# Optimization experiments

Measured on AMD Instinct MI355X. Metric: run time of the kernel, lower is better.

Reference implementation:

```python
import jax, jax.numpy as jnp
import numpy as np

LAMBDA_L1 = 0.5
LAMBDA_SSIM = 0.5
ITERATIONS = 1000
THRESH = 0.01
SUB_N = 50000  # torch caps inlier-check set at 50k points


def setup_inputs() -> dict:
    key = jax.random.key(0)
    k1, k2 = jax.random.split(key)
    H, W = 1024, 2048  # Cityscapes resolution
    rendered_depth = jax.random.uniform(k1, (H, W), jnp.float32, 0.2, 10.0)
    prior_disparity = jax.random.uniform(k2, (H, W), jnp.float32, 0.0, 1.0)
    return {"rendered_depth": rendered_depth, "prior_disparity": prior_disparity}


def _ransac_linear_alignment(x, y, mask, key):
    """Fit y = s*x + t by RANSAC over masked points. x, y, mask are flat [P]."""
    P = x.shape[0]
    num_pts = mask.sum()
    # indices of masked points packed at the front (fixed-shape, jit-safe)
    idx_m = jnp.flatnonzero(mask, size=P, fill_value=0)
    k_pair, k_sub = jax.random.split(key)
    # random point pairs among the first num_pts (masked) entries
    pos = jax.random.randint(k_pair, (ITERATIONS, 2), 0, num_pts)
    pi = idx_m[pos]                                   # [iters, 2]
    x1, x2 = x[pi[:, 0]], x[pi[:, 1]]
    y1, y2 = y[pi[:, 0]], y[pi[:, 1]]
    scales = (y2 - y1) / (x2 - x1 + 1e-8)             # [iters]
    shifts = y1 - scales * x1                         # [iters]
    # subsample inlier-check set (with replacement; torch uses randperm)
    spos = jax.random.randint(k_sub, (SUB_N,), 0, num_pts)
    si = idx_m[spos]
    x_sub, y_sub = x[si], y[si]                       # [SUB_N]
    # dynamic threshold = 0.5 * MAD of masked y
    y_nan = jnp.where(mask, y, jnp.nan)
    med = jnp.nanmedian(y_nan)
    dyn = jnp.nanmedian(jnp.abs(y_nan - med)) * 0.5
    dyn = jnp.where(dyn < 1e-5, THRESH, dyn)
    # all iterations evaluated in parallel: [iters, SUB_N] residuals
    res = jnp.abs(scales[:, None] * x_sub[None, :] + shifts[:, None] - y_sub[None, :])
    counts = (res < dyn).sum(axis=1)
    counts = jnp.where(scales > 0, counts, -1)        # torch skips s <= 0
    best = jnp.argmax(counts)                         # first max == torch's strict-> update
    valid = counts[best] >= 0
    s = jnp.where(valid, scales[best], 1.0)
    t = jnp.where(valid, shifts[best], 0.0)
    # num_pts < 10 fallback
    s = jnp.where(num_pts < 10, 1.0, s)
    t = jnp.where(num_pts < 10, 0.0, t)
    return s, t


def reference(rendered_depth, prior_disparity):
    d_ren = rendered_depth
    d_pri = prior_disparity
    mask = (d_ren > 0.1) & (d_ren < 100.0) & jnp.isfinite(d_ren)
    target_inv_ren = 1.0 / (d_ren + 1e-6)
    n_valid = mask.sum()

    s, t = _ransac_linear_alignment(
        jax.lax.stop_gradient(d_pri).reshape(-1),
        jax.lax.stop_gradient(target_inv_ren).reshape(-1),
        mask.reshape(-1),
        jax.random.key(42),
    )
    aligned_prior_disp = s * d_pri + t
    # masked mean L1 (F.l1_loss over mask-selected elements)
    l1_loss = jnp.sum(jnp.abs(aligned_prior_disp - target_inv_ren) * mask) / jnp.maximum(n_valid, 1)
    total_loss = LAMBDA_L1 * l1_loss + LAMBDA_SSIM * 0.0  # ssim_module=None
    total_loss = jnp.where(n_valid < 100, 0.0, total_loss)  # early-exit branch
    prior_metric_depth = 1.0 / jnp.maximum(jax.lax.stop_gradient(aligned_prior_disp), 1e-4)
    return total_loss, target_inv_ren, prior_metric_depth
```

## Files before the change

### kernel.cpp

```cpp
#include <hip/hip_runtime.h>
#include <stdint.h>
#include <math.h>


#define NT 256
#define GA 128
#define GB 512
#define GC 128
#define GD 512
#define GE 256
#define GF 1024
#define LCAP 262144u

enum : uint32_t {
  W_CNT  = 0,
  W_LOSS = 4,
  W_N    = 6,
  W_VA   = 7, W_VB = 8,
  W_WA   = 9, W_WB = 10,
  W_SB1  = 12,
  W_SB2  = 16,
  W_COUNTS = 20,
  W_G1   = 1024,
  W_G2   = 17408,
  W_ZEND = 33792,
  W_PERC = 33792,
  W_SCALES = 34816,
  W_SHIFTS = 35816,
  W_XSUB = 36816,
  W_YSUB = 86816,
  W_LA1  = 136832,
  W_LB1  = W_LA1 + LCAP,
  W_LA2  = W_LB1 + LCAP,
  W_LB2  = W_LA2 + LCAP
};

__device__ __forceinline__ uint32_t rotl32(uint32_t v, int d) {
  return (v << d) | (v >> (32 - d));
}
__device__ __forceinline__ void tf2x32(uint32_t k0, uint32_t k1,
                                       uint32_t c0, uint32_t c1,
                                       uint32_t& o0, uint32_t& o1) {
  uint32_t ks2 = k0 ^ k1 ^ 0x1BD11BDAu;
  uint32_t x0 = c0 + k0;
  uint32_t x1 = c1 + k1;
#define TFR(r) { x0 += x1; x1 = rotl32(x1, r); x1 ^= x0; }
  TFR(13) TFR(15) TFR(26) TFR(6)
  x0 += k1;  x1 += ks2 + 1u;
  TFR(17) TFR(29) TFR(16) TFR(24)
  x0 += ks2; x1 += k0 + 2u;
  TFR(13) TFR(15) TFR(26) TFR(6)
  x0 += k0;  x1 += k1 + 3u;
  TFR(17) TFR(29) TFR(16) TFR(24)
  x0 += k1;  x1 += ks2 + 4u;
  TFR(13) TFR(15) TFR(26) TFR(6)
  x0 += ks2; x1 += k0 + 5u;
#undef TFR
  o0 = x0; o1 = x1;
}
struct Keys { uint32_t hp0, hp1, lp0, lp1, hs0, hs1, ls0, ls1; };
__device__ __forceinline__ Keys derive_keys() {
  Keys K; uint32_t p0, p1, q0, q1;
  tf2x32(0u, 42u, 0u, 0u, p0, p1);
  tf2x32(0u, 42u, 0u, 1u, q0, q1);
  tf2x32(p0, p1, 0u, 0u, K.hp0, K.hp1);
  tf2x32(p0, p1, 0u, 1u, K.lp0, K.lp1);
  tf2x32(q0, q1, 0u, 0u, K.hs0, K.hs1);
  tf2x32(q0, q1, 0u, 1u, K.ls0, K.ls1);
  return K;
}
__device__ __forceinline__ uint32_t bits32(uint32_t k0, uint32_t k1, uint32_t e) {
  uint32_t a, b; tf2x32(k0, k1, 0u, e, a, b); return a ^ b;
}
__device__ __forceinline__ uint32_t ri_offset(uint32_t hi, uint32_t lo, uint32_t span) {
  uint32_t m = 65536u % span;
  m = (m * m) % span;
  uint32_t off = (hi % span) * m + (lo % span);
  return off % span;
}

__device__ __forceinline__ uint32_t f2u(float f) {
  uint32_t u = __float_as_uint(f);
  return (u & 0x80000000u) ? ~u : (u | 0x80000000u);
}
__device__ __forceinline__ float u2f(uint32_t u) {
  uint32_t v = (u & 0x80000000u) ? (u & 0x7FFFFFFFu) : ~u;
  return __uint_as_float(v);
}
__device__ __forceinline__ uint32_t yval_u(float dv, float& y, bool& m) {
  y = __fdiv_rn(1.0f, __fadd_rn(dv, 1e-6f));
  m = (dv > 0.1f) && (dv < 100.0f) && isfinite(dv);
  return m ? f2u(y) : 0xFFFFFFFFu;
}
__device__ __forceinline__ uint32_t m2w(uint32_t u, float med) {
  return (u != 0xFFFFFFFFu) ? f2u(fabsf(__fsub_rn(u2f(u), med))) : 0xFFFFFFFFu;
}
__device__ __forceinline__ float med_from(const uint32_t* WS) {
  return __fmul_rn(__fadd_rn(u2f(WS[W_VA]), u2f(WS[W_VB])), 0.5f);
}

__device__ __forceinline__ uint32_t block_sum_u32(uint32_t v, uint32_t* wl) {
  const int lane = threadIdx.x & 63, wid = threadIdx.x >> 6;
  for (int off = 32; off > 0; off >>= 1) v += __shfl_down(v, off);
  __syncthreads();
  if (lane == 0) wl[wid] = v;
  __syncthreads();
  return wl[0] + wl[1] + wl[2] + wl[3];
}
__device__ __forceinline__ uint32_t scan_excl(uint32_t local, uint32_t* wl) {
  const int lane = threadIdx.x & 63, wid = threadIdx.x >> 6;
  __syncthreads();
  uint32_t v = local;
#pragma unroll
  for (int off = 1; off < 64; off <<= 1) {
    uint32_t o = __shfl_up(v, off);
    if (lane >= off) v += o;
  }
  if (lane == 63) wl[wid] = v;
  __syncthreads();
  uint32_t base = 0;
  for (int w = 0; w < 4; w++) if (w < wid) base += wl[w];
  return base + v - local;
}

__device__ void g_select2(const uint32_t* __restrict__ G, uint32_t rkA, uint32_t rkB,
                          uint32_t* wl, uint32_t* bc4) {
  const int tid = threadIdx.x;
  if (tid < 4) bc4[tid] = 0u;
  __syncthreads();
  uint32_t local = 0;
  for (int k = 0; k < 64; k++) local += G[tid * 64 + k];
  uint32_t excl = scan_excl(local, wl);
  for (int s = 0; s < 2; s++) {
    uint32_t rk = s ? rkB : rkA;
    if (local > 0 && rk >= excl && rk < excl + local) {
      uint32_t c = excl;
      for (int k = 0; k < 64; k++) {
        uint32_t v = G[tid * 64 + k];
        if (rk < c + v) { bc4[2 * s] = (uint32_t)(tid * 64 + k); bc4[2 * s + 1] = rk - c; break; }
        c += v;
      }
    }
  }
  __syncthreads();
}

__device__ uint32_t select17(const uint32_t* __restrict__ L, uint32_t cnt,
                             uint32_t rk, uint32_t bin14,
                             uint32_t* h512, uint32_t* h256,
                             uint32_t* wl, uint32_t* bc) {
  const int tid = threadIdx.x;
  __syncthreads();
  h512[2 * tid] = 0; h512[2 * tid + 1] = 0; h256[tid] = 0;
  if (tid < 2) bc[tid] = 0u;
  __syncthreads();
  for (uint32_t i = tid; i < cnt; i += NT)
    atomicAdd(&h512[(L[i] >> 8) & 511u], 1u);
  __syncthreads();
  uint32_t a0 = h512[2 * tid], a1 = h512[2 * tid + 1];
  uint32_t local = a0 + a1;
  uint32_t excl = scan_excl(local, wl);
  if (local > 0 && rk >= excl && rk < excl + local) {
    if (rk < excl + a0) { bc[0] = (uint32_t)(2 * tid); bc[1] = rk - excl; }
    else { bc[0] = (uint32_t)(2 * tid + 1); bc[1] = rk - excl - a0; }
  }
  __syncthreads();
  uint32_t binA = bc[0], rk2 = bc[1];
  __syncthreads();
  for (uint32_t i = tid; i < cnt; i += NT) {
    uint32_t v = L[i];
    if (((v >> 8) & 511u) == binA) atomicAdd(&h256[v & 255u], 1u);
  }
  __syncthreads();
  uint32_t l2 = h256[tid];
  uint32_t e2 = scan_excl(l2, wl);
  if (l2 > 0 && rk2 >= e2 && rk2 < e2 + l2) bc[0] = (uint32_t)tid;
  __syncthreads();
  uint32_t binB = bc[0];
  __syncthreads();
  return ((16384u + bin14) << 17) | (binA << 8) | binB;
}

__global__ void k_zero(uint32_t* WS) {
  int i = blockIdx.x * blockDim.x + threadIdx.x;
  if (i < (int)W_ZEND) WS[i] = 0u;
}

__global__ __launch_bounds__(NT) void kA(const float* __restrict__ dren,
                                         uint32_t* __restrict__ WS, int P) {
  const int tid = threadIdx.x, bid = blockIdx.x, gid = bid * NT + tid;
  __shared__ uint32_t lh[8192];
  __shared__ uint32_t wl[4];
  for (int i = tid; i < 8192; i += NT) lh[i] = 0u;
  __syncthreads();
  uint32_t cnt = 0;
  const float4* d4 = (const float4*)dren;
  const int P4 = P >> 2;
  for (int i = gid; i < P4; i += GA * NT) {
    float4 d = d4[i];
    float dc[4] = { d.x, d.y, d.z, d.w };
#pragma unroll
    for (int k = 0; k < 4; k++) {
      float y; bool m;
      uint32_t u = yval_u(dc[k], y, m);
      cnt += m ? 1u : 0u;
      uint32_t bin = (u >> 17) & 16383u;
      atomicAdd(&lh[bin >> 1], 1u << ((bin & 1u) << 4));
    }
  }
  for (int i = (P & ~3) + gid; i < P; i += GA * NT) {
    float y; bool m;
    uint32_t u = yval_u(dren[i], y, m);
    cnt += m ? 1u : 0u;
    uint32_t bin = (u >> 17) & 16383u;
    atomicAdd(&lh[bin >> 1], 1u << ((bin & 1u) << 4));
  }
  uint32_t btot = block_sum_u32(cnt, wl);
  if (tid == 0) WS[W_PERC + bid] = btot;
  __syncthreads();
  for (int w = tid; w < 8192; w += NT) {
    uint32_t pv = lh[w];
    if (pv) {
      uint32_t lo = pv & 0xFFFFu, hi = pv >> 16;
      if (lo) atomicAdd(&WS[W_G1 + 2 * w], lo);
      if (hi) atomicAdd(&WS[W_G1 + 2 * w + 1], hi);
    }
  }
}

__global__ __launch_bounds__(NT) void kB(const float* __restrict__ dren,
                                         const float* __restrict__ dpri,
                                         uint32_t* __restrict__ WS, int P) {
  const int tid = threadIdx.x, bid = blockIdx.x, gid = bid * NT + tid;
  __shared__ uint32_t bufA[4096], bufB[4096];
  __shared__ uint32_t cA, cB, baseA, baseB;
  __shared__ uint32_t wl[4], bc4[4];
  uint32_t local = (tid < GA) ? WS[W_PERC + tid] : 0u;
  const uint32_t n = block_sum_u32(local, wl);
  const uint32_t nn = n ? n : 1u;
  g_select2(WS + W_G1, (nn - 1u) >> 1, nn >> 1, wl, bc4);
  const uint32_t binA1 = bc4[0], binB1 = bc4[2];
  const bool dv1 = (binA1 != binB1);
  if (tid == 0) {
    WS[W_N] = n;
    WS[W_SB1 + 0] = bc4[0]; WS[W_SB1 + 1] = bc4[1];
    WS[W_SB1 + 2] = bc4[2]; WS[W_SB1 + 3] = bc4[3];
    cA = 0; cB = 0;
  }
  __syncthreads();
  {
    uint32_t span = n ? n : 1u;
    if (gid < 1000) {
      Keys K = derive_keys();
      uint32_t hi0 = bits32(K.hp0, K.hp1, (uint32_t)(2 * gid));
      uint32_t lo0 = bits32(K.lp0, K.lp1, (uint32_t)(2 * gid));
      uint32_t hi1 = bits32(K.hp0, K.hp1, (uint32_t)(2 * gid + 1));
      uint32_t lo1 = bits32(K.lp0, K.lp1, (uint32_t)(2 * gid + 1));
      uint32_t i0 = ri_offset(hi0, lo0, span);
      uint32_t i1 = ri_offset(hi1, lo1, span);
      float x1v = dpri[i0], x2v = dpri[i1];
      float y1v = __fdiv_rn(1.0f, __fadd_rn(dren[i0], 1e-6f));
      float y2v = __fdiv_rn(1.0f, __fadd_rn(dren[i1], 1e-6f));
      float sc = __fdiv_rn(__fsub_rn(y2v, y1v),
                           __fadd_rn(__fsub_rn(x2v, x1v), 1e-8f));
      ((float*)WS)[W_SCALES + gid] = sc;
      ((float*)WS)[W_SHIFTS + gid] = __fsub_rn(y1v, __fmul_rn(sc, x1v));
    }
    if (gid < 50000) {
      Keys K = derive_keys();
      uint32_t hi = bits32(K.hs0, K.hs1, (uint32_t)gid);
      uint32_t lo = bits32(K.ls0, K.ls1, (uint32_t)gid);
      uint32_t idx = ri_offset(hi, lo, span);
      ((float*)WS)[W_XSUB + gid] = dpri[idx];
      ((float*)WS)[W_YSUB + gid] = __fdiv_rn(1.0f, __fadd_rn(dren[idx], 1e-6f));
    }
  }
  const float4* d4 = (const float4*)dren;
  const int P4 = P >> 2;
  for (int i = gid; i < P4; i += GB * NT) {
    float4 d = d4[i];
    float dc[4] = { d.x, d.y, d.z, d.w };
#pragma unroll
    for (int k = 0; k < 4; k++) {
      float y; bool m;
      uint32_t u = yval_u(dc[k], y, m);
      uint32_t b = (u >> 17) & 16383u;
      if (b == binA1) { uint32_t j = atomicAdd(&cA, 1u); if (j < 4096u) bufA[j] = u; }
      else if (dv1 && b == binB1) { uint32_t j = atomicAdd(&cB, 1u); if (j < 4096u) bufB[j] = u; }
    }
  }
  for (int i = (P & ~3) + gid; i < P; i += GB * NT) {
    float y; bool m;
    uint32_t u = yval_u(dren[i], y, m);
    uint32_t b = (u >> 17) & 16383u;
    if (b == binA1) { uint32_t j = atomicAdd(&cA, 1u); if (j < 4096u) bufA[j] = u; }
    else if (dv1 && b == binB1) { uint32_t j = atomicAdd(&cB, 1u); if (j < 4096u) bufB[j] = u; }
  }
  __syncthreads();
  if (tid == 0) {
    uint32_t a = cA > 4096u ? 4096u : cA;
    uint32_t b = cB > 4096u ? 4096u : cB;
    cA = a; cB = b;
    baseA = a ? atomicAdd(&WS[W_CNT + 0], a) : 0u;
    baseB = b ? atomicAdd(&WS[W_CNT + 1], b) : 0u;
  }
  __syncthreads();
  for (uint32_t k = tid; k < cA; k += NT)
    if (baseA + k < LCAP) WS[W_LA1 + baseA + k] = bufA[k];
  for (uint32_t k = tid; k < cB; k += NT)
    if (baseB + k < LCAP) WS[W_LB1 + baseB + k] = bufB[k];
}

__global__ __launch_bounds__(NT) void kMed(uint32_t* __restrict__ WS) {
  const int bid = blockIdx.x;
  __shared__ uint32_t h512[512], h256[256];
  __shared__ uint32_t wl[4], bc[2];
  const uint32_t binA1 = WS[W_SB1 + 0], rkA1 = WS[W_SB1 + 1];
  const uint32_t binB1 = WS[W_SB1 + 2], rkB1 = WS[W_SB1 + 3];
  const bool dv1 = (binA1 != binB1);
  uint32_t bin, rk; const uint32_t* L; uint32_t cnt;
  if (bid == 0) {
    bin = binA1; rk = rkA1; L = WS + W_LA1;
    cnt = WS[W_CNT + 0];
  } else {
    bin = dv1 ? binB1 : binA1; rk = rkB1;
    L = dv1 ? (WS + W_LB1) : (WS + W_LA1);
    cnt = dv1 ? WS[W_CNT + 1] : WS[W_CNT + 0];
  }
  if (cnt > LCAP) cnt = LCAP;
  uint32_t v = select17(L, cnt, rk, bin, h512, h256, wl, bc);
  if (threadIdx.x == 0) WS[bid == 0 ? W_VA : W_VB] = v;
}

__global__ __launch_bounds__(NT) void kC(const float* __restrict__ dren,
                                         uint32_t* __restrict__ WS, int P) {
  const int tid = threadIdx.x, bid = blockIdx.x, gid = bid * NT + tid;
  __shared__ uint32_t lh[8192];
  const float med = med_from(WS);
  for (int i = tid; i < 8192; i += NT) lh[i] = 0u;
  __syncthreads();
  const float4* d4 = (const float4*)dren;
  const int P4 = P >> 2;
  for (int i = gid; i < P4; i += GC * NT) {
    float4 d = d4[i];
    float dc[4] = { d.x, d.y, d.z, d.w };
#pragma unroll
    for (int k = 0; k < 4; k++) {
      float y; bool m;
      uint32_t w = m2w(yval_u(dc[k], y, m), med);
      uint32_t bin = (w >> 17) & 16383u;
      atomicAdd(&lh[bin >> 1], 1u << ((bin & 1u) << 4));
    }
  }
  for (int i = (P & ~3) + gid; i < P; i += GC * NT) {
    float y; bool m;
    uint32_t w = m2w(yval_u(dren[i], y, m), med);
    uint32_t bin = (w >> 17) & 16383u;
    atomicAdd(&lh[bin >> 1], 1u << ((bin & 1u) << 4));
  }
  __syncthreads();
  for (int w = tid; w < 8192; w += NT) {
    uint32_t pv = lh[w];
    if (pv) {
      uint32_t lo = pv & 0xFFFFu, hi = pv >> 16;
      if (lo) atomicAdd(&WS[W_G2 + 2 * w], lo);
      if (hi) atomicAdd(&WS[W_G2 + 2 * w + 1], hi);
    }
  }
}

__global__ __launch_bounds__(NT) void kD(const float* __restrict__ dren,
                                         uint32_t* __restrict__ WS, int P) {
  const int tid = threadIdx.x, bid = blockIdx.x, gid = bid * NT + tid;
  __shared__ uint32_t bufA[4096], bufB[4096];
  __shared__ uint32_t cA, cB, baseA, baseB;
  __shared__ uint32_t wl[4], bc4[4];
  const float med = med_from(WS);
  const uint32_t n = WS[W_N];
  const uint32_t nn = n ? n : 1u;
  g_select2(WS + W_G2, (nn - 1u) >> 1, nn >> 1, wl, bc4);
  const uint32_t binA2 = bc4[0], binB2 = bc4[2];
  const bool dv2 = (binA2 != binB2);
  if (tid == 0) {
    WS[W_SB2 + 0] = bc4[0]; WS[W_SB2 + 1] = bc4[1];
    WS[W_SB2 + 2] = bc4[2]; WS[W_SB2 + 3] = bc4[3];
    cA = 0; cB = 0;
  }
  __syncthreads();
  const float4* d4 = (const float4*)dren;
  const int P4 = P >> 2;
  for (int i = gid; i < P4; i += GD * NT) {
    float4 d = d4[i];
    float dc[4] = { d.x, d.y, d.z, d.w };
#pragma unroll
    for (int k = 0; k < 4; k++) {
      float y; bool m;
      uint32_t w = m2w(yval_u(dc[k], y, m), med);
      uint32_t b = (w >> 17) & 16383u;
      if (b == binA2) { uint32_t j = atomicAdd(&cA, 1u); if (j < 4096u) bufA[j] = w; }
      else if (dv2 && b == binB2) { uint32_t j = atomicAdd(&cB, 1u); if (j < 4096u) bufB[j] = w; }
    }
  }
  for (int i = (P & ~3) + gid; i < P; i += GD * NT) {
    float y; bool m;
    uint32_t w = m2w(yval_u(dren[i], y, m), med);
    uint32_t b = (w >> 17) & 16383u;
    if (b == binA2) { uint32_t j = atomicAdd(&cA, 1u); if (j < 4096u) bufA[j] = w; }
    else if (dv2 && b == binB2) { uint32_t j = atomicAdd(&cB, 1u); if (j < 4096u) bufB[j] = w; }
  }
  __syncthreads();
  if (tid == 0) {
    uint32_t a = cA > 4096u ? 4096u : cA;
    uint32_t b = cB > 4096u ? 4096u : cB;
    cA = a; cB = b;
    baseA = a ? atomicAdd(&WS[W_CNT + 2], a) : 0u;
    baseB = b ? atomicAdd(&WS[W_CNT + 3], b) : 0u;
  }
  __syncthreads();
  for (uint32_t k = tid; k < cA; k += NT)
    if (baseA + k < LCAP) WS[W_LA2 + baseA + k] = bufA[k];
  for (uint32_t k = tid; k < cB; k += NT)
    if (baseB + k < LCAP) WS[W_LB2 + baseB + k] = bufB[k];
}

__global__ __launch_bounds__(NT) void kDyn(uint32_t* __restrict__ WS) {
  const int bid = blockIdx.x;
  __shared__ uint32_t h512[512], h256[256];
  __shared__ uint32_t wl[4], bc[2];
  const uint32_t binA2 = WS[W_SB2 + 0], rkA2 = WS[W_SB2 + 1];
  const uint32_t binB2 = WS[W_SB2 + 2], rkB2 = WS[W_SB2 + 3];
  const bool dv2 = (binA2 != binB2);
  uint32_t bin, rk; const uint32_t* L; uint32_t cnt;
  if (bid == 0) {
    bin = binA2; rk = rkA2; L = WS + W_LA2;
    cnt = WS[W_CNT + 2];
  } else {
    bin = dv2 ? binB2 : binA2; rk = rkB2;
    L = dv2 ? (WS + W_LB2) : (WS + W_LA2);
    cnt = dv2 ? WS[W_CNT + 3] : WS[W_CNT + 2];
  }
  if (cnt > LCAP) cnt = LCAP;
  uint32_t v = select17(L, cnt, rk, bin, h512, h256, wl, bc);
  if (threadIdx.x == 0) WS[bid == 0 ? W_WA : W_WB] = v;
}

__global__ __launch_bounds__(NT) void kE(uint32_t* __restrict__ WS) {
  const int tid = threadIdx.x, bid = blockIdx.x;
  __shared__ float lx[200], ly[200];
  float mad = __fmul_rn(__fadd_rn(u2f(WS[W_WA]), u2f(WS[W_WB])), 0.5f);
  float dyn = __fmul_rn(mad, 0.5f);
  if (dyn < 1e-5f) dyn = 0.01f;
  const int e0 = (bid * 50000) / GE, e1 = ((bid + 1) * 50000) / GE;
  const int cnt = e1 - e0;
  const float* x_sub = (const float*)WS + W_XSUB;
  const float* y_sub = (const float*)WS + W_YSUB;
  if (tid < cnt) { lx[tid] = x_sub[e0 + tid]; ly[tid] = y_sub[e0 + tid]; }
  __syncthreads();
  const float* scales = (const float*)WS + W_SCALES;
  const float* shifts = (const float*)WS + W_SHIFTS;
  float ss[4], tt[4]; int c[4];
#pragma unroll
  for (int j = 0; j < 4; j++) {
    int cand = tid + 256 * j;
    ss[j] = (cand < 1000) ? scales[cand] : 0.0f;
    tt[j] = (cand < 1000) ? shifts[cand] : 0.0f;
    c[j] = 0;
  }
  for (int e = 0; e < cnt; e++) {
    float xe = lx[e], ye = ly[e];
#pragma unroll
    for (int j = 0; j < 4; j++) {
      float r = fabsf(__fsub_rn(__fadd_rn(__fmul_rn(ss[j], xe), tt[j]), ye));
      c[j] += (r < dyn) ? 1 : 0;
    }
  }
  int* counts = (int*)WS + W_COUNTS;
#pragma unroll
  for (int j = 0; j < 4; j++) {
    int cand = tid + 256 * j;
    if (cand < 1000 && c[j] > 0) atomicAdd(&counts[cand], c[j]);
  }
}

__global__ __launch_bounds__(NT) void kF(const float* __restrict__ dren,
                                         const float* __restrict__ dpri,
                                         float* __restrict__ out,
                                         uint32_t* __restrict__ WS, int P) {
  const int tid = threadIdx.x, bid = blockIdx.x, gid = bid * NT + tid;
  const int lane = tid & 63, wid = tid >> 6;
  __shared__ int ired[4], iidx[4];
  __shared__ float fbcast[2];
  __shared__ double dred[4];
  {
    const int* counts = (const int*)WS + W_COUNTS;
    const float* scales = (const float*)WS + W_SCALES;
    const float* shifts = (const float*)WS + W_SHIFTS;
    int bcn = -2, bix = 0x7FFFFFFF;
    for (int j = tid; j < 1000; j += NT) {
      int cc = counts[j];
      if (!(scales[j] > 0.0f)) cc = -1;
      if (cc > bcn) { bcn = cc; bix = j; }
    }
    for (int off = 32; off > 0; off >>= 1) {
      int oc = __shfl_down(bcn, off), oi = __shfl_down(bix, off);
      if (oc > bcn || (oc == bcn && oi < bix)) { bcn = oc; bix = oi; }
    }
    if (lane == 0) { ired[wid] = bcn; iidx[wid] = bix; }
    __syncthreads();
    if (tid == 0) {
      for (int w = 1; w < 4; w++) {
        if (ired[w] > ired[0] || (ired[w] == ired[0] && iidx[w] < iidx[0])) {
          ired[0] = ired[w]; iidx[0] = iidx[w];
        }
      }
      bool valid = ired[0] >= 0;
      float s = valid ? scales[iidx[0]] : 1.0f;
      float t = valid ? shifts[iidx[0]] : 0.0f;
      uint32_t n = WS[W_N];
      if (n < 10u) { s = 1.0f; t = 0.0f; }
      fbcast[0] = s; fbcast[1] = t;
    }
    __syncthreads();
  }
  const float s = fbcast[0], t = fbcast[1];
  float* out_y = out + 1;
  float* out_depth = out + 1 + P;
  double acc = 0.0;
  const float4* d4 = (const float4*)dren;
  const float4* p4 = (const float4*)dpri;
  const int P4 = P >> 2;
  for (int i = gid; i < P4; i += GF * NT) {
    float4 d = d4[i], p = p4[i];
    float dc[4] = { d.x, d.y, d.z, d.w };
    float pc[4] = { p.x, p.y, p.z, p.w };
#pragma unroll
    for (int k = 0; k < 4; k++) {
      float yv = __fdiv_rn(1.0f, __fadd_rn(dc[k], 1e-6f));
      out_y[4 * i + k] = yv;
      float al = __fadd_rn(__fmul_rn(s, pc[k]), t);
      out_depth[4 * i + k] = __fdiv_rn(1.0f, fmaxf(al, 1e-4f));
      bool m = (dc[k] > 0.1f) && (dc[k] < 100.0f) && isfinite(dc[k]);
      if (m) acc += (double)fabsf(__fsub_rn(al, yv));
    }
  }
  for (int i = (P & ~3) + gid; i < P; i += GF * NT) {
    float dv = dren[i];
    float yv = __fdiv_rn(1.0f, __fadd_rn(dv, 1e-6f));
    out_y[i] = yv;
    float al = __fadd_rn(__fmul_rn(s, dpri[i]), t);
    out_depth[i] = __fdiv_rn(1.0f, fmaxf(al, 1e-4f));
    bool m = (dv > 0.1f) && (dv < 100.0f) && isfinite(dv);
    if (m) acc += (double)fabsf(__fsub_rn(al, yv));
  }
  for (int off = 32; off > 0; off >>= 1) acc += __shfl_down(acc, off);
  __syncthreads();
  if (lane == 0) dred[wid] = acc;
  __syncthreads();
  if (tid == 0)
    atomicAdd((double*)(WS + W_LOSS), dred[0] + dred[1] + dred[2] + dred[3]);
}

__global__ void kG(const uint32_t* __restrict__ WS, float* __restrict__ out) {
  if (threadIdx.x == 0 && blockIdx.x == 0) {
    double total = *((const double*)(WS + W_LOSS));
    uint32_t n = WS[W_N];
    uint32_t nd = n ? n : 1u;
    float l1 = __fdiv_rn((float)total, (float)nd);
    out[0] = (n < 100u) ? 0.0f : __fmul_rn(0.5f, l1);
  }
}

extern "C" void kernel_launch(void* const* d_in, const int* in_sizes, int n_in,
                              void* d_out, int out_size, void* d_ws, size_t ws_size,
                              hipStream_t stream) {
  const float* d_ren = (const float*)d_in[0];
  const float* d_pri = (const float*)d_in[1];
  float* out = (float*)d_out;
  uint32_t* WS = (uint32_t*)d_ws;
  int P = in_sizes[0];

  k_zero<<<(W_ZEND + NT - 1) / NT, NT, 0, stream>>>(WS);
  kA<<<GA, NT, 0, stream>>>(d_ren, WS, P);
  kB<<<GB, NT, 0, stream>>>(d_ren, d_pri, WS, P);
  kMed<<<2, NT, 0, stream>>>(WS);
  kC<<<GC, NT, 0, stream>>>(d_ren, WS, P);
  kD<<<GD, NT, 0, stream>>>(d_ren, WS, P);
  kDyn<<<2, NT, 0, stream>>>(WS);
  kE<<<GE, NT, 0, stream>>>(WS);
  kF<<<GF, NT, 0, stream>>>(d_ren, d_pri, out, WS, P);
  kG<<<1, 64, 0, stream>>>(WS, out);
}
```

Measured before the change: 226.2 us.

## Fuse median, MAD and final-loss kernels into last-block tails of producers

Removes the separate kMed, kDyn and kG launches. Each producer kernel (kB, kD, kF) now counts finished blocks with an atomic, and the last block to finish does the follow-up select or loss finalization. Writes use atomic exchange and reads use atomic loads, so the last block sees data written by the other blocks. This saves three launch gaps, but the two median selects now run one after another in a single block instead of two blocks in parallel.

Result: slower. 271.4 us (+20.0%).

```diff
diff --git a/kernel.cpp b/kernel.cpp
--- a/kernel.cpp
+++ b/kernel.cpp
@@ -16,10 +16,9 @@
   W_CNT  = 0,
   W_LOSS = 4,
   W_N    = 6,
-  W_VA   = 7, W_VB = 8,
-  W_WA   = 9, W_WB = 10,
-  W_SB1  = 12,
-  W_SB2  = 16,
+  W_MED  = 7,
+  W_DYN  = 8,
+  W_DONEB = 9, W_DONED = 10, W_DONEF = 11,
   W_COUNTS = 20,
   W_G1   = 1024,
   W_G2   = 17408,
@@ -95,8 +94,15 @@
 __device__ __forceinline__ uint32_t m2w(uint32_t u, float med) {
   return (u != 0xFFFFFFFFu) ? f2u(fabsf(__fsub_rn(u2f(u), med))) : 0xFFFFFFFFu;
 }
-__device__ __forceinline__ float med_from(const uint32_t* WS) {
-  return __fmul_rn(__fadd_rn(u2f(WS[W_VA]), u2f(WS[W_VB])), 0.5f);
+
+__device__ __forceinline__ uint32_t aload(const uint32_t* p) {
+  return __hip_atomic_load(p, __ATOMIC_RELAXED, __HIP_MEMORY_SCOPE_AGENT);
+}
+__device__ __forceinline__ uint32_t axchg(uint32_t* p, uint32_t v) {
+  return __hip_atomic_exchange(p, v, __ATOMIC_RELAXED, __HIP_MEMORY_SCOPE_AGENT);
+}
+__device__ __forceinline__ double aloadd(const double* p) {
+  return __hip_atomic_load(p, __ATOMIC_RELAXED, __HIP_MEMORY_SCOPE_AGENT);
 }
 
 __device__ __forceinline__ uint32_t block_sum_u32(uint32_t v, uint32_t* wl) {
@@ -145,17 +151,17 @@
   __syncthreads();
 }
 
-__device__ uint32_t select17(const uint32_t* __restrict__ L, uint32_t cnt,
-                             uint32_t rk, uint32_t bin14,
-                             uint32_t* h512, uint32_t* h256,
-                             uint32_t* wl, uint32_t* bc) {
+__device__ uint32_t select17a(const uint32_t* __restrict__ L, uint32_t cnt,
+                              uint32_t rk, uint32_t bin14,
+                              uint32_t* h512, uint32_t* h256,
+                              uint32_t* wl, uint32_t* bc) {
   const int tid = threadIdx.x;
   __syncthreads();
   h512[2 * tid] = 0; h512[2 * tid + 1] = 0; h256[tid] = 0;
   if (tid < 2) bc[tid] = 0u;
   __syncthreads();
   for (uint32_t i = tid; i < cnt; i += NT)
-    atomicAdd(&h512[(L[i] >> 8) & 511u], 1u);
+    atomicAdd(&h512[(aload(&L[i]) >> 8) & 511u], 1u);
   __syncthreads();
   uint32_t a0 = h512[2 * tid], a1 = h512[2 * tid + 1];
   uint32_t local = a0 + a1;
@@ -168,7 +174,7 @@
   uint32_t binA = bc[0], rk2 = bc[1];
   __syncthreads();
   for (uint32_t i = tid; i < cnt; i += NT) {
-    uint32_t v = L[i];
+    uint32_t v = aload(&L[i]);
     if (((v >> 8) & 511u) == binA) atomicAdd(&h256[v & 255u], 1u);
   }
   __syncthreads();
@@ -235,16 +241,17 @@
   __shared__ uint32_t bufA[4096], bufB[4096];
   __shared__ uint32_t cA, cB, baseA, baseB;
   __shared__ uint32_t wl[4], bc4[4];
+  __shared__ uint32_t h512[512], h256[256];
+  __shared__ int lastB;
   uint32_t local = (tid < GA) ? WS[W_PERC + tid] : 0u;
   const uint32_t n = block_sum_u32(local, wl);
   const uint32_t nn = n ? n : 1u;
   g_select2(WS + W_G1, (nn - 1u) >> 1, nn >> 1, wl, bc4);
-  const uint32_t binA1 = bc4[0], binB1 = bc4[2];
+  const uint32_t binA1 = bc4[0], rkA1 = bc4[1];
+  const uint32_t binB1 = bc4[2], rkB1 = bc4[3];
   const bool dv1 = (binA1 != binB1);
   if (tid == 0) {
     WS[W_N] = n;
-    WS[W_SB1 + 0] = bc4[0]; WS[W_SB1 + 1] = bc4[1];
-    WS[W_SB1 + 2] = bc4[2]; WS[W_SB1 + 3] = bc4[3];
     cA = 0; cB = 0;
   }
   __syncthreads();
@@ -305,38 +312,37 @@
     baseB = b ? atomicAdd(&WS[W_CNT + 1], b) : 0u;
   }
   __syncthreads();
+  uint32_t dummy = 1u;
   for (uint32_t k = tid; k < cA; k += NT)
-    if (baseA + k < LCAP) WS[W_LA1 + baseA + k] = bufA[k];
+    if (baseA + k < LCAP) dummy ^= axchg(&WS[W_LA1 + baseA + k], bufA[k]);
   for (uint32_t k = tid; k < cB; k += NT)
-    if (baseB + k < LCAP) WS[W_LB1 + baseB + k] = bufB[k];
-}
-
-__global__ __launch_bounds__(NT) void kMed(uint32_t* __restrict__ WS) {
-  const int bid = blockIdx.x;
-  __shared__ uint32_t h512[512], h256[256];
-  __shared__ uint32_t wl[4], bc[2];
-  const uint32_t binA1 = WS[W_SB1 + 0], rkA1 = WS[W_SB1 + 1];
-  const uint32_t binB1 = WS[W_SB1 + 2], rkB1 = WS[W_SB1 + 3];
-  const bool dv1 = (binA1 != binB1);
-  uint32_t bin, rk; const uint32_t* L; uint32_t cnt;
-  if (bid == 0) {
-    bin = binA1; rk = rkA1; L = WS + W_LA1;
-    cnt = WS[W_CNT + 0];
+    if (baseB + k < LCAP) dummy ^= axchg(&WS[W_LB1 + baseB + k], bufB[k]);
+  asm volatile("" :: "v"(dummy) : "memory");
+  __syncthreads();
+  if (tid == 0) {
+    uint32_t old = atomicAdd(&WS[W_DONEB], 1u);
+    lastB = (old == (uint32_t)(GB - 1)) ? 1 : 0;
+  }
+  __syncthreads();
+  if (!lastB) return;
+  uint32_t cA1 = aload(&WS[W_CNT + 0]); if (cA1 > LCAP) cA1 = LCAP;
+  uint32_t vA = select17a(WS + W_LA1, cA1, rkA1, binA1, h512, h256, wl, bc4);
+  uint32_t vB;
+  if (dv1) {
+    uint32_t cB1 = aload(&WS[W_CNT + 1]); if (cB1 > LCAP) cB1 = LCAP;
+    vB = select17a(WS + W_LB1, cB1, rkB1, binB1, h512, h256, wl, bc4);
   } else {
-    bin = dv1 ? binB1 : binA1; rk = rkB1;
-    L = dv1 ? (WS + W_LB1) : (WS + W_LA1);
-    cnt = dv1 ? WS[W_CNT + 1] : WS[W_CNT + 0];
-  }
-  if (cnt > LCAP) cnt = LCAP;
-  uint32_t v = select17(L, cnt, rk, bin, h512, h256, wl, bc);
-  if (threadIdx.x == 0) WS[bid == 0 ? W_VA : W_VB] = v;
+    vB = select17a(WS + W_LA1, cA1, rkB1, binA1, h512, h256, wl, bc4);
+  }
+  if (tid == 0)
+    ((float*)WS)[W_MED] = __fmul_rn(__fadd_rn(u2f(vA), u2f(vB)), 0.5f);
 }
 
 __global__ __launch_bounds__(NT) void kC(const float* __restrict__ dren,
                                          uint32_t* __restrict__ WS, int P) {
   const int tid = threadIdx.x, bid = blockIdx.x, gid = bid * NT + tid;
   __shared__ uint32_t lh[8192];
-  const float med = med_from(WS);
+  const float med = ((const float*)WS)[W_MED];
   for (int i = tid; i < 8192; i += NT) lh[i] = 0u;
   __syncthreads();
   const float4* d4 = (const float4*)dren;
@@ -375,17 +381,16 @@
   __shared__ uint32_t bufA[4096], bufB[4096];
   __shared__ uint32_t cA, cB, baseA, baseB;
   __shared__ uint32_t wl[4], bc4[4];
-  const float med = med_from(WS);
+  __shared__ uint32_t h512[512], h256[256];
+  __shared__ int lastD;
+  const float med = ((const float*)WS)[W_MED];
   const uint32_t n = WS[W_N];
   const uint32_t nn = n ? n : 1u;
   g_select2(WS + W_G2, (nn - 1u) >> 1, nn >> 1, wl, bc4);
-  const uint32_t binA2 = bc4[0], binB2 = bc4[2];
+  const uint32_t binA2 = bc4[0], rkA2 = bc4[1];
+  const uint32_t binB2 = bc4[2], rkB2 = bc4[3];
   const bool dv2 = (binA2 != binB2);
-  if (tid == 0) {
-    WS[W_SB2 + 0] = bc4[0]; WS[W_SB2 + 1] = bc4[1];
-    WS[W_SB2 + 2] = bc4[2]; WS[W_SB2 + 3] = bc4[3];
-    cA = 0; cB = 0;
-  }
+  if (tid == 0) { cA = 0; cB = 0; }
   __syncthreads();
   const float4* d4 = (const float4*)dren;
   const int P4 = P >> 2;
@@ -417,39 +422,40 @@
     baseB = b ? atomicAdd(&WS[W_CNT + 3], b) : 0u;
   }
   __syncthreads();
+  uint32_t dummy = 1u;
   for (uint32_t k = tid; k < cA; k += NT)
-    if (baseA + k < LCAP) WS[W_LA2 + baseA + k] = bufA[k];
+    if (baseA + k < LCAP) dummy ^= axchg(&WS[W_LA2 + baseA + k], bufA[k]);
   for (uint32_t k = tid; k < cB; k += NT)
-    if (baseB + k < LCAP) WS[W_LB2 + baseB + k] = bufB[k];
-}
-
-__global__ __launch_bounds__(NT) void kDyn(uint32_t* __restrict__ WS) {
-  const int bid = blockIdx.x;
-  __shared__ uint32_t h512[512], h256[256];
-  __shared__ uint32_t wl[4], bc[2];
-  const uint32_t binA2 = WS[W_SB2 + 0], rkA2 = WS[W_SB2 + 1];
-  const uint32_t binB2 = WS[W_SB2 + 2], rkB2 = WS[W_SB2 + 3];
-  const bool dv2 = (binA2 != binB2);
-  uint32_t bin, rk; const uint32_t* L; uint32_t cnt;
-  if (bid == 0) {
-    bin = binA2; rk = rkA2; L = WS + W_LA2;
-    cnt = WS[W_CNT + 2];
+    if (baseB + k < LCAP) dummy ^= axchg(&WS[W_LB2 + baseB + k], bufB[k]);
+  asm volatile("" :: "v"(dummy) : "memory");
+  __syncthreads();
+  if (tid == 0) {
+    uint32_t old = atomicAdd(&WS[W_DONED], 1u);
+    lastD = (old == (uint32_t)(GD - 1)) ? 1 : 0;
+  }
+  __syncthreads();
+  if (!lastD) return;
+  uint32_t cA2 = aload(&WS[W_CNT + 2]); if (cA2 > LCAP) cA2 = LCAP;
+  uint32_t wA = select17a(WS + W_LA2, cA2, rkA2, binA2, h512, h256, wl, bc4);
+  uint32_t wB;
+  if (dv2) {
+    uint32_t cB2 = aload(&WS[W_CNT + 3]); if (cB2 > LCAP) cB2 = LCAP;
+    wB = select17a(WS + W_LB2, cB2, rkB2, binB2, h512, h256, wl, bc4);
   } else {
-    bin = dv2 ? binB2 : binA2; rk = rkB2;
-    L = dv2 ? (WS + W_LB2) : (WS + W_LA2);
-    cnt = dv2 ? WS[W_CNT + 3] : WS[W_CNT + 2];
-  }
-  if (cnt > LCAP) cnt = LCAP;
-  uint32_t v = select17(L, cnt, rk, bin, h512, h256, wl, bc);
-  if (threadIdx.x == 0) WS[bid == 0 ? W_WA : W_WB] = v;
+    wB = select17a(WS + W_LA2, cA2, rkB2, binA2, h512, h256, wl, bc4);
+  }
+  if (tid == 0) {
+    float mad = __fmul_rn(__fadd_rn(u2f(wA), u2f(wB)), 0.5f);
+    float dyn = __fmul_rn(mad, 0.5f);
+    if (dyn < 1e-5f) dyn = 0.01f;
+    ((float*)WS)[W_DYN] = dyn;
+  }
 }
 
 __global__ __launch_bounds__(NT) void kE(uint32_t* __restrict__ WS) {
   const int tid = threadIdx.x, bid = blockIdx.x;
   __shared__ float lx[200], ly[200];
-  float mad = __fmul_rn(__fadd_rn(u2f(WS[W_WA]), u2f(WS[W_WB])), 0.5f);
-  float dyn = __fmul_rn(mad, 0.5f);
-  if (dyn < 1e-5f) dyn = 0.01f;
+  const float dyn = ((const float*)WS)[W_DYN];
   const int e0 = (bid * 50000) / GE, e1 = ((bid + 1) * 50000) / GE;
   const int cnt = e1 - e0;
   const float* x_sub = (const float*)WS + W_XSUB;
@@ -491,6 +497,7 @@
   __shared__ int ired[4], iidx[4];
   __shared__ float fbcast[2];
   __shared__ double dred[4];
+  __shared__ int lastF;
   {
     const int* counts = (const int*)WS + W_COUNTS;
     const float* scales = (const float*)WS + W_SCALES;
@@ -556,13 +563,17 @@
   __syncthreads();
   if (lane == 0) dred[wid] = acc;
   __syncthreads();
-  if (tid == 0)
-    atomicAdd((double*)(WS + W_LOSS), dred[0] + dred[1] + dred[2] + dred[3]);
-}
-
-__global__ void kG(const uint32_t* __restrict__ WS, float* __restrict__ out) {
-  if (threadIdx.x == 0 && blockIdx.x == 0) {
-    double total = *((const double*)(WS + W_LOSS));
+  if (tid == 0) {
+    double olds = atomicAdd((double*)(WS + W_LOSS),
+                            dred[0] + dred[1] + dred[2] + dred[3]);
+    uint32_t lo = (uint32_t)__double_as_longlong(olds);
+    asm volatile("" :: "v"(lo) : "memory");
+    uint32_t old = atomicAdd(&WS[W_DONEF], 1u);
+    lastF = (old == (uint32_t)(GF - 1)) ? 1 : 0;
+  }
+  __syncthreads();
+  if (lastF && tid == 0) {
+    double total = aloadd((const double*)(WS + W_LOSS));
     uint32_t n = WS[W_N];
     uint32_t nd = n ? n : 1u;
     float l1 = __fdiv_rn((float)total, (float)nd);
@@ -582,11 +593,8 @@
   k_zero<<<(W_ZEND + NT - 1) / NT, NT, 0, stream>>>(WS);
   kA<<<GA, NT, 0, stream>>>(d_ren, WS, P);
   kB<<<GB, NT, 0, stream>>>(d_ren, d_pri, WS, P);
-  kMed<<<2, NT, 0, stream>>>(WS);
   kC<<<GC, NT, 0, stream>>>(d_ren, WS, P);
   kD<<<GD, NT, 0, stream>>>(d_ren, WS, P);
-  kDyn<<<2, NT, 0, stream>>>(WS);
   kE<<<GE, NT, 0, stream>>>(WS);
   kF<<<GF, NT, 0, stream>>>(d_ren, d_pri, out, WS, P);
-  kG<<<1, 64, 0, stream>>>(WS, out);
-}
+}
```

## Fold median selection kernels into consumers and use wave-aggregated histogram atomics

Applied to the files above, without the earlier changes.

Removes the separate two-block kMed and kDyn launches. Every block of kC and kE now redundantly runs the radix-select over the candidate lists to get the median or MAD itself, and kC publishes the median for kD. The select histogram also switches from per-thread LDS atomics to ballot-based wave aggregation with 8-way unrolled loads. The aim is to cut two launches and the serial gaps between them, at the cost of repeating the selection work in every block and adding a serialized prefix to each block of kC and kE.

After: 284.8 us. 1.26x slower.

```diff
diff --git a/kernel.cpp b/kernel.cpp
--- a/kernel.cpp
+++ b/kernel.cpp
@@ -16,10 +16,9 @@
   W_CNT  = 0,
   W_LOSS = 4,
   W_N    = 6,
-  W_VA   = 7, W_VB = 8,
-  W_WA   = 9, W_WB = 10,
-  W_SB1  = 12,
-  W_SB2  = 16,
+  W_MED  = 7,
+  W_SB1  = 8,
+  W_SB2  = 12,
   W_COUNTS = 20,
   W_G1   = 1024,
   W_G2   = 17408,
@@ -95,9 +94,6 @@
 __device__ __forceinline__ uint32_t m2w(uint32_t u, float med) {
   return (u != 0xFFFFFFFFu) ? f2u(fabsf(__fsub_rn(u2f(u), med))) : 0xFFFFFFFFu;
 }
-__device__ __forceinline__ float med_from(const uint32_t* WS) {
-  return __fmul_rn(__fadd_rn(u2f(WS[W_VA]), u2f(WS[W_VB])), 0.5f);
-}
 
 __device__ __forceinline__ uint32_t block_sum_u32(uint32_t v, uint32_t* wl) {
   const int lane = threadIdx.x & 63, wid = threadIdx.x >> 6;
@@ -145,17 +141,46 @@
   __syncthreads();
 }
 
-__device__ uint32_t select17(const uint32_t* __restrict__ L, uint32_t cnt,
-                             uint32_t rk, uint32_t bin14,
-                             uint32_t* h512, uint32_t* h256,
-                             uint32_t* wl, uint32_t* bc) {
+template <int BITS>
+__device__ __forceinline__ void wave_hist_add(uint32_t* hist, uint32_t bin, bool part) {
+  const int lane = threadIdx.x & 63;
+  unsigned long long act = __ballot(part ? 1 : 0);
+  unsigned long long m = act;
+#pragma unroll
+  for (int b = 0; b < BITS; b++) {
+    bool bit = part && ((bin >> b) & 1u);
+    unsigned long long vote = __ballot(bit ? 1 : 0);
+    m &= ((bin >> b) & 1u) ? vote : ~vote;
+  }
+  if (part) {
+    int leader = __ffsll(m) - 1;
+    if (lane == leader) atomicAdd(&hist[bin], (uint32_t)__popcll(m));
+  }
+}
+
+__device__ uint32_t select17i(const uint32_t* __restrict__ L, uint32_t cnt,
+                              uint32_t rk, uint32_t bin14,
+                              uint32_t* h512, uint32_t* h256,
+                              uint32_t* wl, uint32_t* bc) {
   const int tid = threadIdx.x;
   __syncthreads();
   h512[2 * tid] = 0; h512[2 * tid + 1] = 0; h256[tid] = 0;
   if (tid < 2) bc[tid] = 0u;
   __syncthreads();
-  for (uint32_t i = tid; i < cnt; i += NT)
-    atomicAdd(&h512[(L[i] >> 8) & 511u], 1u);
+  {
+    uint32_t i = (uint32_t)tid;
+    while (i + 7u * NT < cnt) {
+      uint32_t v[8];
+#pragma unroll
+      for (int k = 0; k < 8; k++) v[k] = L[i + (uint32_t)k * NT];
+#pragma unroll
+      for (int k = 0; k < 8; k++)
+        wave_hist_add<9>(h512, (v[k] >> 8) & 511u, true);
+      i += 8u * NT;
+    }
+    for (; i < cnt; i += NT)
+      wave_hist_add<9>(h512, (L[i] >> 8) & 511u, true);
+  }
   __syncthreads();
   uint32_t a0 = h512[2 * tid], a1 = h512[2 * tid + 1];
   uint32_t local = a0 + a1;
@@ -167,9 +192,21 @@
   __syncthreads();
   uint32_t binA = bc[0], rk2 = bc[1];
   __syncthreads();
-  for (uint32_t i = tid; i < cnt; i += NT) {
-    uint32_t v = L[i];
-    if (((v >> 8) & 511u) == binA) atomicAdd(&h256[v & 255u], 1u);
+  {
+    uint32_t i = (uint32_t)tid;
+    while (i + 7u * NT < cnt) {
+      uint32_t v[8];
+#pragma unroll
+      for (int k = 0; k < 8; k++) v[k] = L[i + (uint32_t)k * NT];
+#pragma unroll
+      for (int k = 0; k < 8; k++)
+        wave_hist_add<8>(h256, v[k] & 255u, ((v[k] >> 8) & 511u) == binA);
+      i += 8u * NT;
+    }
+    for (; i < cnt; i += NT) {
+      uint32_t v = L[i];
+      wave_hist_add<8>(h256, v & 255u, ((v >> 8) & 511u) == binA);
+    }
   }
   __syncthreads();
   uint32_t l2 = h256[tid];
@@ -311,32 +348,27 @@
     if (baseB + k < LCAP) WS[W_LB1 + baseB + k] = bufB[k];
 }
 
-__global__ __launch_bounds__(NT) void kMed(uint32_t* __restrict__ WS) {
-  const int bid = blockIdx.x;
+__global__ __launch_bounds__(NT) void kC(const float* __restrict__ dren,
+                                         uint32_t* __restrict__ WS, int P) {
+  const int tid = threadIdx.x, bid = blockIdx.x, gid = bid * NT + tid;
+  __shared__ uint32_t lh[8192];
   __shared__ uint32_t h512[512], h256[256];
   __shared__ uint32_t wl[4], bc[2];
   const uint32_t binA1 = WS[W_SB1 + 0], rkA1 = WS[W_SB1 + 1];
   const uint32_t binB1 = WS[W_SB1 + 2], rkB1 = WS[W_SB1 + 3];
   const bool dv1 = (binA1 != binB1);
-  uint32_t bin, rk; const uint32_t* L; uint32_t cnt;
-  if (bid == 0) {
-    bin = binA1; rk = rkA1; L = WS + W_LA1;
-    cnt = WS[W_CNT + 0];
+  uint32_t cA1 = WS[W_CNT + 0]; if (cA1 > LCAP) cA1 = LCAP;
+  uint32_t vA = select17i(WS + W_LA1, cA1, rkA1, binA1, h512, h256, wl, bc);
+  uint32_t vB;
+  if (dv1) {
+    uint32_t cB1 = WS[W_CNT + 1]; if (cB1 > LCAP) cB1 = LCAP;
+    vB = select17i(WS + W_LB1, cB1, rkB1, binB1, h512, h256, wl, bc);
   } else {
-    bin = dv1 ? binB1 : binA1; rk = rkB1;
-    L = dv1 ? (WS + W_LB1) : (WS + W_LA1);
-    cnt = dv1 ? WS[W_CNT + 1] : WS[W_CNT + 0];
-  }
-  if (cnt > LCAP) cnt = LCAP;
-  uint32_t v = select17(L, cnt, rk, bin, h512, h256, wl, bc);
-  if (threadIdx.x == 0) WS[bid == 0 ? W_VA : W_VB] = v;
-}
-
-__global__ __launch_bounds__(NT) void kC(const float* __restrict__ dren,
-                                         uint32_t* __restrict__ WS, int P) {
-  const int tid = threadIdx.x, bid = blockIdx.x, gid = bid * NT + tid;
-  __shared__ uint32_t lh[8192];
-  const float med = med_from(WS);
+    vB = select17i(WS + W_LA1, cA1, rkB1, binA1, h512, h256, wl, bc);
+  }
+  const float med = __fmul_rn(__fadd_rn(u2f(vA), u2f(vB)), 0.5f);
+  if (tid == 0) ((float*)WS)[W_MED] = med;
+  __syncthreads();
   for (int i = tid; i < 8192; i += NT) lh[i] = 0u;
   __syncthreads();
   const float4* d4 = (const float4*)dren;
@@ -375,7 +407,7 @@
   __shared__ uint32_t bufA[4096], bufB[4096];
   __shared__ uint32_t cA, cB, baseA, baseB;
   __shared__ uint32_t wl[4], bc4[4];
-  const float med = med_from(WS);
+  const float med = ((const float*)WS)[W_MED];
   const uint32_t n = WS[W_N];
   const uint32_t nn = n ? n : 1u;
   g_select2(WS + W_G2, (nn - 1u) >> 1, nn >> 1, wl, bc4);
@@ -423,31 +455,24 @@
     if (baseB + k < LCAP) WS[W_LB2 + baseB + k] = bufB[k];
 }
 
-__global__ __launch_bounds__(NT) void kDyn(uint32_t* __restrict__ WS) {
-  const int bid = blockIdx.x;
+__global__ __launch_bounds__(NT) void kE(uint32_t* __restrict__ WS) {
+  const int tid = threadIdx.x, bid = blockIdx.x;
   __shared__ uint32_t h512[512], h256[256];
   __shared__ uint32_t wl[4], bc[2];
+  __shared__ float lx[200], ly[200];
   const uint32_t binA2 = WS[W_SB2 + 0], rkA2 = WS[W_SB2 + 1];
   const uint32_t binB2 = WS[W_SB2 + 2], rkB2 = WS[W_SB2 + 3];
   const bool dv2 = (binA2 != binB2);
-  uint32_t bin, rk; const uint32_t* L; uint32_t cnt;
-  if (bid == 0) {
-    bin = binA2; rk = rkA2; L = WS + W_LA2;
-    cnt = WS[W_CNT + 2];
+  uint32_t cA2 = WS[W_CNT + 2]; if (cA2 > LCAP) cA2 = LCAP;
+  uint32_t wA = select17i(WS + W_LA2, cA2, rkA2, binA2, h512, h256, wl, bc);
+  uint32_t wB;
+  if (dv2) {
+    uint32_t cB2 = WS[W_CNT + 3]; if (cB2 > LCAP) cB2 = LCAP;
+    wB = select17i(WS + W_LB2, cB2, rkB2, binB2, h512, h256, wl, bc);
   } else {
-    bin = dv2 ? binB2 : binA2; rk = rkB2;
-    L = dv2 ? (WS + W_LB2) : (WS + W_LA2);
-    cnt = dv2 ? WS[W_CNT + 3] : WS[W_CNT + 2];
-  }
-  if (cnt > LCAP) cnt = LCAP;
-  uint32_t v = select17(L, cnt, rk, bin, h512, h256, wl, bc);
-  if (threadIdx.x == 0) WS[bid == 0 ? W_WA : W_WB] = v;
-}
-
-__global__ __launch_bounds__(NT) void kE(uint32_t* __restrict__ WS) {
-  const int tid = threadIdx.x, bid = blockIdx.x;
-  __shared__ float lx[200], ly[200];
-  float mad = __fmul_rn(__fadd_rn(u2f(WS[W_WA]), u2f(WS[W_WB])), 0.5f);
+    wB = select17i(WS + W_LA2, cA2, rkB2, binA2, h512, h256, wl, bc);
+  }
+  float mad = __fmul_rn(__fadd_rn(u2f(wA), u2f(wB)), 0.5f);
   float dyn = __fmul_rn(mad, 0.5f);
   if (dyn < 1e-5f) dyn = 0.01f;
   const int e0 = (bid * 50000) / GE, e1 = ((bid + 1) * 50000) / GE;
@@ -582,10 +607,8 @@
   k_zero<<<(W_ZEND + NT - 1) / NT, NT, 0, stream>>>(WS);
   kA<<<GA, NT, 0, stream>>>(d_ren, WS, P);
   kB<<<GB, NT, 0, stream>>>(d_ren, d_pri, WS, P);
-  kMed<<<2, NT, 0, stream>>>(WS);
   kC<<<GC, NT, 0, stream>>>(d_ren, WS, P);
   kD<<<GD, NT, 0, stream>>>(d_ren, WS, P);
-  kDyn<<<2, NT, 0, stream>>>(WS);
   kE<<<GE, NT, 0, stream>>>(WS);
   kF<<<GF, NT, 0, stream>>>(d_ren, d_pri, out, WS, P);
   kG<<<1, 64, 0, stream>>>(WS, out);
```
